# Performance work log

Measured on AMD Instinct MI355X. Metric: run time of the kernel, lower is better.

The kernel has to match this reference:

```python
import jax, jax.numpy as jnp
import numpy as np

B, C, H, W = 8, 256, 96, 96
HEADS, K = 8, 7  # kernel_size 7 -> 49 neighbors per query
HD = C // HEADS


def setup_inputs() -> dict:
    key = jax.random.key(0)
    ks = jax.random.split(key, 6)
    s = 0.02
    return {
        "x": jax.random.normal(ks[0], (B, C, H, W), jnp.float32),
        "wq": jax.random.normal(ks[1], (C, C), jnp.float32) * s,
        "wk": jax.random.normal(ks[2], (C, C), jnp.float32) * s,
        "wv": jax.random.normal(ks[3], (C, C), jnp.float32) * s,
        "w_proj": jax.random.normal(ks[4], (C, C), jnp.float32) * s,
        "b_proj": jnp.zeros((C,), jnp.float32),
        "rpb": jax.random.normal(ks[5], (HEADS, 2 * K - 1, 2 * K - 1), jnp.float32) * 0.02,
    }


def reference(x, wq, wk, wv, w_proj, b_proj, rpb):
    b, c, h, w = x.shape
    hd = c // HEADS
    scale = hd ** -0.5
    r = K // 2

    def conv1x1(wmat, t):
        return jnp.einsum('oc,bchw->bohw', wmat, t)

    def split_heads(t):
        # b (hd c) h w -> b hd h w c
        return t.reshape(b, HEADS, hd, h, w).transpose(0, 1, 3, 4, 2)

    q = split_heads(conv1x1(wq, x)) * scale
    k = split_heads(conv1x1(wk, x))
    v = split_heads(conv1x1(wv, x))

    # NATTEN neighborhood: window of size K starting at s_i, clamped to image
    s_h = jnp.clip(jnp.arange(h) - r, 0, h - K)  # (h,)
    s_w = jnp.clip(jnp.arange(w) - r, 0, w - K)  # (w,)
    off = jnp.arange(K)
    # relative-position-bias indices: (key_pos - query_pos) + (K-1) in [0, 2K-2]
    bi = s_h[:, None] + off[None, :] - jnp.arange(h)[:, None] + (K - 1)  # (h,K)
    bj = s_w[:, None] + off[None, :] - jnp.arange(w)[:, None] + (K - 1)  # (w,K)
    bias = rpb[:, bi[:, None, :, None], bj[None, :, None, :]]  # (heads,h,w,K,K)

    # QK: loop over the K*K fixed offsets (structural, not data-dim loop)
    logits = []
    for ki in range(K):
        k_r = k[:, :, s_h + ki]  # (b,heads,h,w,hd)
        for kj in range(K):
            k_sh = k_r[:, :, :, s_w + kj]
            logits.append(jnp.einsum('bhijc,bhijc->bhij', q, k_sh))
    attn = jnp.stack(logits, axis=-1).reshape(b, HEADS, h, w, K, K)
    attn = attn + bias[None]
    attn = jax.nn.softmax(attn.reshape(b, HEADS, h, w, K * K), axis=-1)
    attn = attn.reshape(b, HEADS, h, w, K, K)

    # AV: accumulate over the same offsets
    out = jnp.zeros_like(q)
    for ki in range(K):
        v_r = v[:, :, s_h + ki]
        for kj in range(K):
            v_sh = v_r[:, :, :, s_w + kj]
            out = out + attn[..., ki, kj, None] * v_sh

    # b hd h w f -> b h w (hd f), then proj (Linear dim->dim), back to b c h w
    merged = out.transpose(0, 2, 3, 1, 4).reshape(b, h, w, HEADS * hd)
    y = jnp.einsum('bhwc,oc->bhwo', merged, w_proj) + b_proj
    return y.transpose(0, 3, 1, 2)
```

## Files before the change

kernel.cpp:

```cpp
#include <hip/hip_runtime.h>
#include <stdint.h>

#define BATCH  8
#define CH     256
#define HH     96
#define WW     96
#define NHEADS 8
#define HD     32
#define KS     7
#define HWP    (HH*WW)
#define SCALE  0.17677669529663687f

#define HSTR  24
#define HSLOT 576
#define VSTR  584
#define NT    11
#define PBS   200

typedef unsigned short ushort_t;
typedef unsigned short us8 __attribute__((ext_vector_type(8)));
typedef short s8v __attribute__((ext_vector_type(8)));
typedef float f4v __attribute__((ext_vector_type(4)));

__device__ __forceinline__ ushort_t f2bf(float f){
  unsigned int u = __float_as_uint(f);
  u = u + 0x7fffu + ((u >> 16) & 1u);
  return (ushort_t)(u >> 16);
}
__device__ __forceinline__ float bflo(unsigned int u){ return __uint_as_float(u << 16); }

__device__ __forceinline__ void gload_lds16(const void* g, void* l){
  __builtin_amdgcn_global_load_lds(
      (const __attribute__((address_space(1))) void*)g,
      (__attribute__((address_space(3))) void*)l, 16, 0, 0);
}

__global__ __launch_bounds__(256) void wcvt_kernel(
    const float* __restrict__ wq, const float* __restrict__ wk,
    const float* __restrict__ wv, const float* __restrict__ wp,
    ushort_t* __restrict__ wbf)
{
  int i = blockIdx.x*256 + threadIdx.x;
  int mat = i >> 16;
  int off = i & 65535;
  const float* src = (mat==0) ? wq : (mat==1) ? wk : (mat==2) ? wv : wp;
  wbf[i] = f2bf(src[off]);
}

__global__ __launch_bounds__(256) void xpose_kernel(
    const float* __restrict__ x, ushort_t* __restrict__ xT)
{
  __shared__ unsigned int tile[32][33];
  int p0 = blockIdx.x * 64;
  int c0 = blockIdx.y * 32;
  int b  = blockIdx.z;
  int tid = threadIdx.x;
  int tx = tid & 31, ty = tid >> 5;
  const float* xb = x + ((size_t)(b*CH + c0))*HWP;
  #pragma unroll
  for (int r = 0; r < 4; r++){
    int c = r*8 + ty;
    float2 v = *(const float2*)(xb + (size_t)c*HWP + p0 + tx*2);
    tile[c][tx] = (unsigned int)f2bf(v.x) | ((unsigned int)f2bf(v.y) << 16);
  }
  __syncthreads();
  int pv = tid >> 2, cq = tid & 3;
  ushort_t tmp[8];
  #pragma unroll
  for (int s = 0; s < 8; s++){
    unsigned int w = tile[cq*8 + s][pv >> 1];
    tmp[s] = (ushort_t)((pv & 1) ? (w >> 16) : (w & 0xffffu));
  }
  *(us8*)(xT + ((size_t)(b*HWP + p0 + pv))*CH + c0 + cq*8) = *(us8*)tmp;
}

__global__ __launch_bounds__(256) void qkv_gemm(
    const ushort_t* __restrict__ xT, const ushort_t* __restrict__ wbf,
    ushort_t* __restrict__ qb, ushort_t* __restrict__ kb, ushort_t* __restrict__ vb)
{
  __shared__ ushort_t As[128*32];
  __shared__ ushort_t Bs[128*32];
  int m0 = blockIdx.x * 128;
  int n0 = blockIdx.y * 128;
  int b  = blockIdx.z / 3;
  int mat= blockIdx.z % 3;
  int tid = threadIdx.x;
  int wave = tid >> 6, lane = tid & 63;
  const ushort_t* Abase = xT + ((size_t)(b*HWP + m0))*CH;
  const ushort_t* Bbase = wbf + mat*65536 + n0*CH;

  f4v acc[4][4];
  #pragma unroll
  for (int i=0;i<4;i++)
    #pragma unroll
    for (int j=0;j<4;j++) acc[i][j] = (f4v){0.f,0.f,0.f,0.f};

  int wm = wave & 1, wn = wave >> 1;
  int lane16 = lane & 15, quad = lane >> 4;
  int lrow = lane >> 2, lchunk = lane & 3;

  for (int kt = 0; kt < 8; kt++){
    #pragma unroll
    for (int inst = 0; inst < 2; inst++){
      int row0 = wave*32 + inst*16;
      gload_lds16(Abase + (size_t)(row0 + lrow)*CH + kt*32 + lchunk*8, &As[row0*32]);
      gload_lds16(Bbase + (size_t)(row0 + lrow)*CH + kt*32 + lchunk*8, &Bs[row0*32]);
    }
    __syncthreads();
    s8v a[4], bf[4];
    #pragma unroll
    for (int mi=0;mi<4;mi++) a[mi]  = *(const s8v*)&As[(wm*64 + mi*16 + lane16)*32 + quad*8];
    #pragma unroll
    for (int ni=0;ni<4;ni++) bf[ni] = *(const s8v*)&Bs[(wn*64 + ni*16 + lane16)*32 + quad*8];
    #pragma unroll
    for (int mi=0;mi<4;mi++)
      #pragma unroll
      for (int ni=0;ni<4;ni++)
        acc[mi][ni] = __builtin_amdgcn_mfma_f32_16x16x32_bf16(a[mi], bf[ni], acc[mi][ni], 0, 0, 0);
    __syncthreads();
  }

  ushort_t* dst = (mat==0) ? qb : (mat==1) ? kb : vb;
  float sc = (mat==0) ? SCALE : 1.0f;
  size_t obase = (size_t)b * NHEADS * HWP * HD;
  #pragma unroll
  for (int mi=0;mi<4;mi++){
    #pragma unroll
    for (int ni=0;ni<4;ni++){
      int o = n0 + wn*64 + ni*16 + lane16;
      int head = o >> 5, hd = o & 31;
      #pragma unroll
      for (int r=0;r<4;r++){
        int m = m0 + wm*64 + mi*16 + quad*4 + r;
        dst[obase + ((size_t)head*HWP + m)*HD + hd] = f2bf(acc[mi][ni][r] * sc);
      }
    }
  }
}

__global__ __launch_bounds__(512) void attn_kernel(
    const ushort_t* __restrict__ qb, const ushort_t* __restrict__ kb,
    const ushort_t* __restrict__ vb, const float* __restrict__ rpb,
    ushort_t* __restrict__ merged)
{
  __shared__ ushort_t kT[4*HSLOT*8];
  __shared__ ushort_t vTT[32*VSTR];
  __shared__ ushort_t Pbuf[8][16*PBS];
  __shared__ float rpsPad[224];

  int tb = blockIdx.x;
  int i0 = (tb/6)*16, j0 = (tb%6)*16;
  int head = blockIdx.y, b = blockIdx.z;
  int tid = threadIdx.x;
  int wave = tid >> 6, lane = tid & 63;
  int lane16 = lane & 15, quad = lane >> 4;

  int hs0 = max(i0-3, 0);
  int ws0 = max(j0-3, 0);
  size_t kvbase = ((size_t)(b*NHEADS + head)) * HWP * HD;

  for (int pb = wave; pb < 9; pb += 8){
    int s = pb*64 + lane;
    int xx = s >> 3; int r = (xx*171) >> 9;
    int c24 = s - r*24; int cc = min(c24, 21);
    int gr = min(hs0 + r,  HH-1);
    int gc = min(ws0 + cc, WW-1);
    const ushort_t* gp = kb + kvbase + (size_t)(gr*WW + gc)*HD;
    #pragma unroll
    for (int c = 0; c < 4; c++)
      gload_lds16(gp + c*8, &kT[c*(HSLOT*8) + pb*64*8]);
  }
  #pragma unroll
  for (int it = 0; it < 5; it++){
    int idx = it*512 + tid;
    if (idx < 2304){
      int pix = idx >> 2, c = idx & 3;
      int xx = pix >> 3; int r = (xx*171) >> 9;
      int c24 = pix - r*24; int cc = min(c24, 21);
      int gr = min(hs0 + r,  HH-1);
      int gc = min(ws0 + cc, WW-1);
      us8 vv = *(const us8*)(vb + kvbase + (size_t)(gr*WW + gc)*HD + c*8);
      #pragma unroll
      for (int e = 0; e < 8; e++) vTT[(c*8+e)*VSTR + pix] = vv[e];
    }
  }
  if (tid < 224) rpsPad[tid] = (tid >= 16 && tid < 185) ? rpb[head*169 + tid - 16] : 0.f;

  s8v qfragA = *(const s8v*)(qb + kvbase + (size_t)((i0 + wave*2    )*WW + j0 + lane16)*HD + quad*8);
  s8v qfragB = *(const s8v*)(qb + kvbase + (size_t)((i0 + wave*2 + 1)*WW + j0 + lane16)*HD + quad*8);

  unsigned int pk[22];
  #pragma unroll
  for (int ii = 0; ii < 22; ii++){
    unsigned int w = 0;
    #pragma unroll
    for (int h = 0; h < 2; h++){
      int idx = ii*2 + h;
      int tt = idx >> 2, r = idx & 3;
      int n = tt*16 + quad*4 + r;
      int xx = n >> 3; int rk = (xx*171) >> 9;
      int col = n - rk*24;
      int code = (rk >= 7) ? 255 : col;
      int m13c = rk*13 + col;
      w |= (unsigned)((code & 255) | (m13c << 8)) << (h*16);
    }
    pk[ii] = w;
  }

  int j = j0 + lane16;
  int cs_g = min(max(j-3, 0), WW-KS);
  unsigned int cs = (unsigned)(cs_g - ws0);
  int lanePart = ws0 - j + 6 + 16;

  __syncthreads();

  int iA = i0 + wave*2, iB = iA + 1;
  int siA_g = min(max(iA-3, 0), HH-KS);
  int siB_g = min(max(iB-3, 0), HH-KS);
  int rowBaseA = (siA_g - iA + 6)*13 + lanePart;
  int rowBaseB = (siB_g - iB + 6)*13 + lanePart;
  int kbaseA = (siA_g - hs0)*HSTR;
  int kbaseB = (siB_g - hs0)*HSTR;

  f4v cA[NT], cB[NT];
  #pragma unroll
  for (int tt = 0; tt < NT; tt++){
    s8v af = *(const s8v*)&kT[quad*(HSLOT*8) + (kbaseA + tt*16 + lane16)*8];
    cA[tt] = __builtin_amdgcn_mfma_f32_16x16x32_bf16(af, qfragA, (f4v){0.f,0.f,0.f,0.f}, 0, 0, 0);
  }
  #pragma unroll
  for (int tt = 0; tt < NT; tt++){
    s8v af = *(const s8v*)&kT[quad*(HSLOT*8) + (kbaseB + tt*16 + lane16)*8];
    cB[tt] = __builtin_amdgcn_mfma_f32_16x16x32_bf16(af, qfragB, (f4v){0.f,0.f,0.f,0.f}, 0, 0, 0);
  }

  float sA = 0.f, sB = 0.f;
  #pragma unroll
  for (int tt = 0; tt < NT; tt++){
    #pragma unroll
    for (int r = 0; r < 4; r++){
      int idx = tt*4 + r;
      unsigned int ex = pk[idx >> 1] >> ((idx & 1)*16);
      unsigned int col = ex & 255u;
      int m13c = (int)((ex >> 8) & 255u);
      float eA = __expf(cA[tt][r] + rpsPad[rowBaseA + m13c]);
      float eB = __expf(cB[tt][r] + rpsPad[rowBaseB + m13c]);
      bool valid = ((col - cs) <= 6u);
      eA = valid ? eA : 0.f;
      eB = valid ? eB : 0.f;
      sA += eA; sB += eB;
      cA[tt][r] = eA; cB[tt][r] = eB;
    }
  }
  sA += __shfl_xor(sA, 16); sA += __shfl_xor(sA, 32);
  sB += __shfl_xor(sB, 16); sB += __shfl_xor(sB, 32);
  float invA = 1.0f / sA, invB = 1.0f / sB;

  ushort_t* pw = &Pbuf[wave][lane16*PBS];

  #pragma unroll
  for (int tt = 0; tt < NT; tt++){
    uint2 pp;
    pp.x = (unsigned)f2bf(cA[tt][0]*invA) | ((unsigned)f2bf(cA[tt][1]*invA) << 16);
    pp.y = (unsigned)f2bf(cA[tt][2]*invA) | ((unsigned)f2bf(cA[tt][3]*invA) << 16);
    *(uint2*)&pw[tt*16 + quad*4] = pp;
  }
  *(uint2*)&pw[NT*16 + quad*4] = (uint2){0u, 0u};

  f4v o0 = {0.f,0.f,0.f,0.f}, o1 = {0.f,0.f,0.f,0.f};
  #pragma unroll
  for (int kk = 0; kk < 6; kk++){
    s8v pa = *(const s8v*)&Pbuf[wave][lane16*PBS + kk*32 + quad*8];
    s8v v0 = *(const s8v*)&vTT[lane16*VSTR      + kbaseA + kk*32 + quad*8];
    s8v v1 = *(const s8v*)&vTT[(16+lane16)*VSTR + kbaseA + kk*32 + quad*8];
    o0 = __builtin_amdgcn_mfma_f32_16x16x32_bf16(pa, v0, o0, 0, 0, 0);
    o1 = __builtin_amdgcn_mfma_f32_16x16x32_bf16(pa, v1, o1, 0, 0, 0);
  }
  {
    size_t mb = ((size_t)(b*HWP) + (size_t)iA*WW + j0 + quad*4)*CH + head*HD + lane16;
    #pragma unroll
    for (int r = 0; r < 4; r++){
      merged[mb + (size_t)r*CH]      = f2bf(o0[r]);
      merged[mb + (size_t)r*CH + 16] = f2bf(o1[r]);
    }
  }

  #pragma unroll
  for (int tt = 0; tt < NT; tt++){
    uint2 pp;
    pp.x = (unsigned)f2bf(cB[tt][0]*invB) | ((unsigned)f2bf(cB[tt][1]*invB) << 16);
    pp.y = (unsigned)f2bf(cB[tt][2]*invB) | ((unsigned)f2bf(cB[tt][3]*invB) << 16);
    *(uint2*)&pw[tt*16 + quad*4] = pp;
  }
  *(uint2*)&pw[NT*16 + quad*4] = (uint2){0u, 0u};

  f4v p0 = {0.f,0.f,0.f,0.f}, p1 = {0.f,0.f,0.f,0.f};
  #pragma unroll
  for (int kk = 0; kk < 6; kk++){
    s8v pa = *(const s8v*)&Pbuf[wave][lane16*PBS + kk*32 + quad*8];
    s8v v0 = *(const s8v*)&vTT[lane16*VSTR      + kbaseB + kk*32 + quad*8];
    s8v v1 = *(const s8v*)&vTT[(16+lane16)*VSTR + kbaseB + kk*32 + quad*8];
    p0 = __builtin_amdgcn_mfma_f32_16x16x32_bf16(pa, v0, p0, 0, 0, 0);
    p1 = __builtin_amdgcn_mfma_f32_16x16x32_bf16(pa, v1, p1, 0, 0, 0);
  }
  {
    size_t mb = ((size_t)(b*HWP) + (size_t)iB*WW + j0 + quad*4)*CH + head*HD + lane16;
    #pragma unroll
    for (int r = 0; r < 4; r++){
      merged[mb + (size_t)r*CH]      = f2bf(p0[r]);
      merged[mb + (size_t)r*CH + 16] = f2bf(p1[r]);
    }
  }
}

__global__ __launch_bounds__(256) void proj_gemm(
    const ushort_t* __restrict__ merged, const ushort_t* __restrict__ wbf,
    const float* __restrict__ bias, float* __restrict__ y)
{
  __shared__ ushort_t As[128*32];
  __shared__ ushort_t Bs[128*32];
  int m0 = blockIdx.x * 128;
  int n0 = blockIdx.y * 128;
  int b  = blockIdx.z;
  int tid = threadIdx.x;
  int wave = tid >> 6, lane = tid & 63;
  const ushort_t* Abase = merged + ((size_t)(b*HWP + m0))*CH;
  const ushort_t* Bbase = wbf + 3*65536 + n0*CH;

  f4v acc[4][4];
  #pragma unroll
  for (int i=0;i<4;i++)
    #pragma unroll
    for (int j=0;j<4;j++) acc[i][j] = (f4v){0.f,0.f,0.f,0.f};

  int wm = wave & 1, wn = wave >> 1;
  int lane16 = lane & 15, quad = lane >> 4;
  int lrow = lane >> 2, lchunk = lane & 3;

  for (int kt = 0; kt < 8; kt++){
    #pragma unroll
    for (int inst = 0; inst < 2; inst++){
      int row0 = wave*32 + inst*16;
      gload_lds16(Abase + (size_t)(row0 + lrow)*CH + kt*32 + lchunk*8, &As[row0*32]);
      gload_lds16(Bbase + (size_t)(row0 + lrow)*CH + kt*32 + lchunk*8, &Bs[row0*32]);
    }
    __syncthreads();
    s8v a[4], bf[4];
    #pragma unroll
    for (int mi=0;mi<4;mi++) a[mi]  = *(const s8v*)&As[(wm*64 + mi*16 + lane16)*32 + quad*8];
    #pragma unroll
    for (int ni=0;ni<4;ni++) bf[ni] = *(const s8v*)&Bs[(wn*64 + ni*16 + lane16)*32 + quad*8];
    #pragma unroll
    for (int mi=0;mi<4;mi++)
      #pragma unroll
      for (int ni=0;ni<4;ni++)
        acc[mi][ni] = __builtin_amdgcn_mfma_f32_16x16x32_bf16(a[mi], bf[ni], acc[mi][ni], 0, 0, 0);
    __syncthreads();
  }

  #pragma unroll
  for (int mi=0;mi<4;mi++){
    #pragma unroll
    for (int ni=0;ni<4;ni++){
      int o = n0 + wn*64 + ni*16 + lane16;
      float bo = bias[o];
      int mb = m0 + wm*64 + mi*16 + quad*4;
      float4 val;
      val.x = acc[mi][ni][0] + bo;
      val.y = acc[mi][ni][1] + bo;
      val.z = acc[mi][ni][2] + bo;
      val.w = acc[mi][ni][3] + bo;
      *(float4*)&y[((size_t)(b*CH + o))*HWP + mb] = val;
    }
  }
}

extern "C" void kernel_launch(void* const* d_in, const int* in_sizes, int n_in,
                              void* d_out, int out_size, void* d_ws, size_t ws_size,
                              hipStream_t stream)
{
  const float* x   = (const float*)d_in[0];
  const float* wq  = (const float*)d_in[1];
  const float* wk  = (const float*)d_in[2];
  const float* wv  = (const float*)d_in[3];
  const float* wp  = (const float*)d_in[4];
  const float* bp  = (const float*)d_in[5];
  const float* rpb = (const float*)d_in[6];
  float* y = (float*)d_out;

  const size_t SZ = (size_t)BATCH * HWP * CH * 2;
  char* ws = (char*)d_ws;
  ushort_t* xT     = (ushort_t*)ws;  ws += SZ;
  ushort_t* qbuf   = (ushort_t*)ws;  ws += SZ;
  ushort_t* kbuf   = (ushort_t*)ws;  ws += SZ;
  ushort_t* vbuf   = (ushort_t*)ws;  ws += SZ;
  ushort_t* merged = (ushort_t*)ws;  ws += SZ;
  ushort_t* wbf    = (ushort_t*)ws;  ws += (size_t)4*65536*2;
  if (ws_size < (size_t)5*SZ + 4*65536*2) return;

  wcvt_kernel <<<dim3(1024),        dim3(256), 0, stream>>>(wq, wk, wv, wp, wbf);
  xpose_kernel<<<dim3(144, 8, 8),   dim3(256), 0, stream>>>(x, xT);
  qkv_gemm    <<<dim3(72, 2, 24),   dim3(256), 0, stream>>>(xT, wbf, qbuf, kbuf, vbuf);
  attn_kernel <<<dim3(36, 8, 8),    dim3(512), 0, stream>>>(qbuf, kbuf, vbuf, rpb, merged);
  proj_gemm   <<<dim3(72, 2, 8),    dim3(256), 0, stream>>>(merged, wbf, bp, y);
}
```

Measured before the change: 311.9 us.

## Keep full-K A tile resident in LDS and loop over all N columns per block

Both GEMMs now load the whole 128x256 A row block into LDS once, using an XOR swizzle against bank conflicts, and reuse it across all 256 output columns. In the QKV GEMM it is also reused across all three weight matrices. Blocks grow to 512 threads and the grid shrinks, cutting redundant A reads from global memory. The cost is a 64KB+16KB LDS footprint that limits occupancy, fewer blocks, and serialized per-matrix loops with no double buffering.

```diff
diff --git a/kernel.cpp b/kernel.cpp
--- a/kernel.cpp
+++ b/kernel.cpp
@@ -74,65 +74,78 @@
   *(us8*)(xT + ((size_t)(b*HWP + p0 + pv))*CH + c0 + cq*8) = *(us8*)tmp;
 }
 
-__global__ __launch_bounds__(256) void qkv_gemm(
+__global__ __launch_bounds__(512) void qkv_gemm(
     const ushort_t* __restrict__ xT, const ushort_t* __restrict__ wbf,
     ushort_t* __restrict__ qb, ushort_t* __restrict__ kb, ushort_t* __restrict__ vb)
 {
-  __shared__ ushort_t As[128*32];
-  __shared__ ushort_t Bs[128*32];
+  __shared__ ushort_t As[128*256];
+  __shared__ ushort_t Bs[256*32];
   int m0 = blockIdx.x * 128;
-  int n0 = blockIdx.y * 128;
-  int b  = blockIdx.z / 3;
-  int mat= blockIdx.z % 3;
+  int b  = blockIdx.y;
   int tid = threadIdx.x;
   int wave = tid >> 6, lane = tid & 63;
+  int lane16 = lane & 15, quad = lane >> 4;
+  int wm = wave & 1, wn = wave >> 1;
+
   const ushort_t* Abase = xT + ((size_t)(b*HWP + m0))*CH;
-  const ushort_t* Bbase = wbf + mat*65536 + n0*CH;
-
-  f4v acc[4][4];
-  #pragma unroll
-  for (int i=0;i<4;i++)
-    #pragma unroll
-    for (int j=0;j<4;j++) acc[i][j] = (f4v){0.f,0.f,0.f,0.f};
-
-  int wm = wave & 1, wn = wave >> 1;
-  int lane16 = lane & 15, quad = lane >> 4;
-  int lrow = lane >> 2, lchunk = lane & 3;
-
-  for (int kt = 0; kt < 8; kt++){
-    #pragma unroll
-    for (int inst = 0; inst < 2; inst++){
-      int row0 = wave*32 + inst*16;
-      gload_lds16(Abase + (size_t)(row0 + lrow)*CH + kt*32 + lchunk*8, &As[row0*32]);
-      gload_lds16(Bbase + (size_t)(row0 + lrow)*CH + kt*32 + lchunk*8, &Bs[row0*32]);
-    }
-    __syncthreads();
-    s8v a[4], bf[4];
-    #pragma unroll
-    for (int mi=0;mi<4;mi++) a[mi]  = *(const s8v*)&As[(wm*64 + mi*16 + lane16)*32 + quad*8];
-    #pragma unroll
-    for (int ni=0;ni<4;ni++) bf[ni] = *(const s8v*)&Bs[(wn*64 + ni*16 + lane16)*32 + quad*8];
-    #pragma unroll
-    for (int mi=0;mi<4;mi++)
+
+  #pragma unroll
+  for (int it = 0; it < 8; it++){
+    int q = it*512 + tid;
+    int m = q >> 5, cs = q & 31;
+    const ushort_t* src = Abase + (size_t)m*CH + ((cs ^ (m & 7))*8);
+    gload_lds16(src, &As[(it*512 + wave*64)*8]);
+  }
+
+  size_t obase = (size_t)b * NHEADS * HWP * HD;
+
+  for (int mat = 0; mat < 3; mat++){
+    const ushort_t* Bbase = wbf + mat*65536;
+    f4v acc[4][4];
+    #pragma unroll
+    for (int i=0;i<4;i++)
+      #pragma unroll
+      for (int j=0;j<4;j++) acc[i][j] = (f4v){0.f,0.f,0.f,0.f};
+
+    for (int kt = 0; kt < 8; kt++){
+      #pragma unroll
+      for (int it = 0; it < 2; it++){
+        int q = it*512 + tid;
+        const ushort_t* src = Bbase + (size_t)(q >> 2)*CH + kt*32 + (q & 3)*8;
+        gload_lds16(src, &Bs[(it*512 + wave*64)*8]);
+      }
+      __syncthreads();
+      s8v a[4], bf[4];
+      int cc = kt*4 + quad;
+      #pragma unroll
+      for (int mi=0;mi<4;mi++){
+        int m = wm*64 + mi*16 + lane16;
+        a[mi] = *(const s8v*)&As[(m*32 + (cc ^ (m & 7)))*8];
+      }
       #pragma unroll
       for (int ni=0;ni<4;ni++)
-        acc[mi][ni] = __builtin_amdgcn_mfma_f32_16x16x32_bf16(a[mi], bf[ni], acc[mi][ni], 0, 0, 0);
-    __syncthreads();
-  }
-
-  ushort_t* dst = (mat==0) ? qb : (mat==1) ? kb : vb;
-  float sc = (mat==0) ? SCALE : 1.0f;
-  size_t obase = (size_t)b * NHEADS * HWP * HD;
-  #pragma unroll
-  for (int mi=0;mi<4;mi++){
-    #pragma unroll
-    for (int ni=0;ni<4;ni++){
-      int o = n0 + wn*64 + ni*16 + lane16;
-      int head = o >> 5, hd = o & 31;
-      #pragma unroll
-      for (int r=0;r<4;r++){
-        int m = m0 + wm*64 + mi*16 + quad*4 + r;
-        dst[obase + ((size_t)head*HWP + m)*HD + hd] = f2bf(acc[mi][ni][r] * sc);
+        bf[ni] = *(const s8v*)&Bs[(wn*64 + ni*16 + lane16)*32 + quad*8];
+      #pragma unroll
+      for (int mi=0;mi<4;mi++)
+        #pragma unroll
+        for (int ni=0;ni<4;ni++)
+          acc[mi][ni] = __builtin_amdgcn_mfma_f32_16x16x32_bf16(a[mi], bf[ni], acc[mi][ni], 0, 0, 0);
+      __syncthreads();
+    }
+
+    ushort_t* dst = (mat==0) ? qb : (mat==1) ? kb : vb;
+    float sc = (mat==0) ? SCALE : 1.0f;
+    #pragma unroll
+    for (int mi=0;mi<4;mi++){
+      #pragma unroll
+      for (int ni=0;ni<4;ni++){
+        int o = wn*64 + ni*16 + lane16;
+        int head = o >> 5, hd = o & 31;
+        #pragma unroll
+        for (int r=0;r<4;r++){
+          int m = m0 + wm*64 + mi*16 + quad*4 + r;
+          dst[obase + ((size_t)head*HWP + m)*HD + hd] = f2bf(acc[mi][ni][r] * sc);
+        }
       }
     }
   }
@@ -313,19 +326,29 @@
   }
 }
 
-__global__ __launch_bounds__(256) void proj_gemm(
+__global__ __launch_bounds__(512) void proj_gemm(
     const ushort_t* __restrict__ merged, const ushort_t* __restrict__ wbf,
     const float* __restrict__ bias, float* __restrict__ y)
 {
-  __shared__ ushort_t As[128*32];
-  __shared__ ushort_t Bs[128*32];
+  __shared__ ushort_t As[128*256];
+  __shared__ ushort_t Bs[256*32];
   int m0 = blockIdx.x * 128;
-  int n0 = blockIdx.y * 128;
-  int b  = blockIdx.z;
+  int b  = blockIdx.y;
   int tid = threadIdx.x;
   int wave = tid >> 6, lane = tid & 63;
+  int lane16 = lane & 15, quad = lane >> 4;
+  int wm = wave & 1, wn = wave >> 1;
+
   const ushort_t* Abase = merged + ((size_t)(b*HWP + m0))*CH;
-  const ushort_t* Bbase = wbf + 3*65536 + n0*CH;
+  const ushort_t* Bbase = wbf + 3*65536;
+
+  #pragma unroll
+  for (int it = 0; it < 8; it++){
+    int q = it*512 + tid;
+    int m = q >> 5, cs = q & 31;
+    const ushort_t* src = Abase + (size_t)m*CH + ((cs ^ (m & 7))*8);
+    gload_lds16(src, &As[(it*512 + wave*64)*8]);
+  }
 
   f4v acc[4][4];
   #pragma unroll
@@ -333,23 +356,24 @@
     #pragma unroll
     for (int j=0;j<4;j++) acc[i][j] = (f4v){0.f,0.f,0.f,0.f};
 
-  int wm = wave & 1, wn = wave >> 1;
-  int lane16 = lane & 15, quad = lane >> 4;
-  int lrow = lane >> 2, lchunk = lane & 3;
-
   for (int kt = 0; kt < 8; kt++){
     #pragma unroll
-    for (int inst = 0; inst < 2; inst++){
-      int row0 = wave*32 + inst*16;
-      gload_lds16(Abase + (size_t)(row0 + lrow)*CH + kt*32 + lchunk*8, &As[row0*32]);
-      gload_lds16(Bbase + (size_t)(row0 + lrow)*CH + kt*32 + lchunk*8, &Bs[row0*32]);
+    for (int it = 0; it < 2; it++){
+      int q = it*512 + tid;
+      const ushort_t* src = Bbase + (size_t)(q >> 2)*CH + kt*32 + (q & 3)*8;
+      gload_lds16(src, &Bs[(it*512 + wave*64)*8]);
     }
     __syncthreads();
     s8v a[4], bf[4];
-    #pragma unroll
-    for (int mi=0;mi<4;mi++) a[mi]  = *(const s8v*)&As[(wm*64 + mi*16 + lane16)*32 + quad*8];
-    #pragma unroll
-    for (int ni=0;ni<4;ni++) bf[ni] = *(const s8v*)&Bs[(wn*64 + ni*16 + lane16)*32 + quad*8];
+    int cc = kt*4 + quad;
+    #pragma unroll
+    for (int mi=0;mi<4;mi++){
+      int m = wm*64 + mi*16 + lane16;
+      a[mi] = *(const s8v*)&As[(m*32 + (cc ^ (m & 7)))*8];
+    }
+    #pragma unroll
+    for (int ni=0;ni<4;ni++)
+      bf[ni] = *(const s8v*)&Bs[(wn*64 + ni*16 + lane16)*32 + quad*8];
     #pragma unroll
     for (int mi=0;mi<4;mi++)
       #pragma unroll
@@ -362,7 +386,7 @@
   for (int mi=0;mi<4;mi++){
     #pragma unroll
     for (int ni=0;ni<4;ni++){
-      int o = n0 + wn*64 + ni*16 + lane16;
+      int o = wn*64 + ni*16 + lane16;
       float bo = bias[o];
       int mb = m0 + wm*64 + mi*16 + quad*4;
       float4 val;
@@ -400,7 +424,7 @@
 
   wcvt_kernel <<<dim3(1024),        dim3(256), 0, stream>>>(wq, wk, wv, wp, wbf);
   xpose_kernel<<<dim3(144, 8, 8),   dim3(256), 0, stream>>>(x, xT);
-  qkv_gemm    <<<dim3(72, 2, 24),   dim3(256), 0, stream>>>(xT, wbf, qbuf, kbuf, vbuf);
+  qkv_gemm    <<<dim3(72, 8),       dim3(512), 0, stream>>>(xT, wbf, qbuf, kbuf, vbuf);
   attn_kernel <<<dim3(36, 8, 8),    dim3(512), 0, stream>>>(qbuf, kbuf, vbuf, rpb, merged);
-  proj_gemm   <<<dim3(72, 2, 8),    dim3(256), 0, stream>>>(merged, wbf, bp, y);
-}
+  proj_gemm   <<<dim3(72, 8),       dim3(512), 0, stream>>>(merged, wbf, bp, y);
+}
```

Measured after the change: 345.3 us. 1.11x slower.
